# Optimization experiments

Measured on AMD Instinct MI355X. Metric: run time of the kernel, lower is better.

## Reference

```python
import jax, jax.numpy as jnp
import numpy as np

B = 262144
IN = 89          # obs(39) + one-hot task(50)
H = 64           # hidden_size
OUT = 8          # output_size
T = 50           # num_tasks


def setup_inputs() -> dict:
    key = jax.random.key(0)
    ks = jax.random.split(key, 10)
    s = 1.0 / np.sqrt(H)
    inputs = jax.random.normal(ks[0], (B, IN), dtype=jnp.float32)
    task_indices = jax.random.randint(ks[1], (B,), 0, T, dtype=jnp.int32)
    # trunk: 3 Linear+Tanh layers
    W0 = jax.random.normal(ks[2], (IN, H), dtype=jnp.float32) / np.sqrt(IN)
    b0 = jnp.zeros((H,), dtype=jnp.float32)
    W1 = jax.random.normal(ks[3], (H, H), dtype=jnp.float32) * s
    b1 = jnp.zeros((H,), dtype=jnp.float32)
    W2 = jax.random.normal(ks[4], (H, H), dtype=jnp.float32) * s
    b2 = jnp.zeros((H,), dtype=jnp.float32)
    # per-task output heads: num_task_layers=1 -> single Linear (no tanh)
    head_W = jax.random.normal(ks[5], (T, H, OUT), dtype=jnp.float32) * s
    head_b = jnp.zeros((T, OUT), dtype=jnp.float32)
    return {"inputs": inputs, "task_indices": task_indices,
            "W0": W0, "b0": b0, "W1": W1, "b1": b1, "W2": W2, "b2": b2,
            "head_W": head_W, "head_b": head_b}


def reference(inputs, task_indices, W0, b0, W1, b1, W2, b2, head_W, head_b):
    # Shared trunk: Linear + Tanh x3
    h = jnp.tanh(inputs @ W0 + b0)   # [B, H]
    h = jnp.tanh(h @ W1 + b1)
    h = jnp.tanh(h @ W2 + b2)
    # MoE-style dispatch/combine: gather per-sample head weights and apply.
    # Mathematically identical to partitioning by task, applying each head,
    # and scattering results back to original order.
    Wg = head_W[task_indices]        # [B, H, OUT]
    bg = head_b[task_indices]        # [B, OUT]
    out = jnp.einsum('bh,bho->bo', h, Wg) + bg  # [B, OUT]
    return out
```

## Files before the change

### kernel.cpp

```cpp
#include <hip/hip_runtime.h>
#include <stdint.h>
#include <stddef.h>


typedef _Float16 half8 __attribute__((ext_vector_type(8)));
typedef _Float16 half4 __attribute__((ext_vector_type(4)));
typedef _Float16 half2v __attribute__((ext_vector_type(2)));
typedef float    f32x4 __attribute__((ext_vector_type(4)));

constexpr int BN = 262144, INF = 89, HID = 64, OUTF = 8, NTASK = 50;
constexpr int NTHR = 512;
constexpr int NW   = 8;
constexpr int ROWS = 256;
constexpr int HP   = 72;
constexpr int WLF  = 14336;

constexpr int W0F_OFF = 0;
constexpr int W1F_OFF = 12288;
constexpr int W2F_OFF = 20480;
constexpr int HWT_OFF = 28672;

__device__ __forceinline__ float fast_tanh(float v) {
    float e = __expf(2.0f * v);
    return 1.0f - 2.0f * __builtin_amdgcn_rcpf(e + 1.0f);
}

__device__ __forceinline__ float dot2acc(half2v a, half2v b, float c) {
#if __has_builtin(__builtin_amdgcn_fdot2)
    return __builtin_amdgcn_fdot2(a, b, c, false);
#else
    return fmaf((float)a[0], (float)b[0], fmaf((float)a[1], (float)b[1], c));
#endif
}

__global__ void prep_kernel(const float* __restrict__ W0, const float* __restrict__ W1,
                            const float* __restrict__ W2, const float* __restrict__ hW,
                            _Float16* __restrict__ ws) {
    const int tid = blockIdx.x * blockDim.x + threadIdx.x;
    const int stride = gridDim.x * blockDim.x;
    _Float16* w0f = ws + W0F_OFF / 2;
    _Float16* w1f = ws + W1F_OFF / 2;
    _Float16* w2f = ws + W2F_OFF / 2;
    _Float16* hwt = ws + HWT_OFF / 2;
    for (int i = tid; i < 3 * 4 * 64 * 8; i += stride) {
        int j = i & 7, l = (i >> 3) & 63, fk = i >> 9;
        int kk = fk >> 2, ft = fk & 3;
        int n = ft * 16 + (l & 15);
        int g = l >> 4;
        bool tail = (kk == 2 && g == 3);
        int k = (tail ? 81 : kk * 32 + g * 8) + j;
        float wv = W0[k * HID + n];
        if (tail && j < 7) wv = 0.0f;
        w0f[i] = (_Float16)wv;
    }
    for (int i = tid; i < 2 * 4 * 64 * 8; i += stride) {
        int j = i & 7, l = (i >> 3) & 63, fk = i >> 9;
        int kk = fk >> 2, ft = fk & 3;
        int n = ft * 16 + (l & 15);
        int k = kk * 32 + (l >> 4) * 8 + j;
        w1f[i] = (_Float16)W1[k * HID + n];
        w2f[i] = (_Float16)W2[k * HID + n];
    }
    for (int i = tid; i < NTASK * OUTF * HID; i += stride) {
        int t = i / (OUTF * HID), rem = i % (OUTF * HID);
        int o = rem / HID, k = rem % HID;
        hwt[i] = (_Float16)hW[(size_t)t * (HID * OUTF) + k * OUTF + o];
    }
}

__global__ __launch_bounds__(NTHR, 4) void mtn_mfma_kernel(
    const float* __restrict__ x,
    const int*   __restrict__ task,
    const float* __restrict__ b0, const float* __restrict__ b1,
    const float* __restrict__ b2,
    const float* __restrict__ hB,
    const _Float16* __restrict__ ws,
    float* __restrict__ out)
{
    __shared__ __align__(16) _Float16 wl[WLF];
    __shared__ __align__(16) _Float16 hs[NW][32][HP];

    const int t = threadIdx.x;
    const int w = t >> 6;
    const int l = t & 63;
    const int c = l & 15;
    const int g = l >> 4;
    const int waveRow = blockIdx.x * ROWS + w * 32;

    const _Float16* hwt = ws + HWT_OFF / 2;

    {
        const float4* src = reinterpret_cast<const float4*>(ws);
        float4* dst = reinterpret_cast<float4*>(wl);
        #pragma unroll
        for (int i = 0; i < 3; ++i) dst[t + i * NTHR] = src[t + i * NTHR];
        if (t < 1792 - 3 * NTHR) dst[t + 3 * NTHR] = src[t + 3 * NTHR];
    }

    const int k0_2 = (g == 3) ? 81 : 64 + g * 8;
    half8 xf[3][2];
    #pragma unroll
    for (int bt = 0; bt < 2; ++bt) {
        const float* xr = x + (size_t)(waveRow + bt * 16 + c) * INF;
        #pragma unroll
        for (int kk = 0; kk < 3; ++kk) {
            const int k0 = (kk == 2) ? k0_2 : kk * 32 + g * 8;
            float v[8];
            __builtin_memcpy(v, xr + k0, 32);
            half8 hb;
            #pragma unroll
            for (int i2 = 0; i2 < 8; ++i2) hb[i2] = (_Float16)v[i2];
            xf[kk][bt] = hb;
        }
    }

    const int jr = l >> 3, jo = l & 7;
    int   tks[4];
    float hBv[4];
    #pragma unroll
    for (int it = 0; it < 4; ++it)
        tks[it] = task[waveRow + it * 8 + jr];
    #pragma unroll
    for (int it = 0; it < 4; ++it)
        hBv[it] = hB[tks[it] * OUTF + jo];

    __syncthreads();

    const _Float16* w0l = wl;
    const _Float16* w1l = wl + W1F_OFF / 2;
    const _Float16* w2l = wl + W2F_OFF / 2;

    f32x4 acc[4][2];

    #pragma unroll
    for (int ft = 0; ft < 4; ++ft) {
        f32x4 bv = *(const f32x4*)(b0 + ft * 16 + g * 4);
        acc[ft][0] = bv; acc[ft][1] = bv;
    }
    #pragma unroll
    for (int kk = 0; kk < 3; ++kk)
        #pragma unroll
        for (int ft = 0; ft < 4; ++ft) {
            half8 af = *(const half8*)(w0l + ((kk * 4 + ft) * 64 + l) * 8);
            acc[ft][0] = __builtin_amdgcn_mfma_f32_16x16x32_f16(af, xf[kk][0], acc[ft][0], 0, 0, 0);
            acc[ft][1] = __builtin_amdgcn_mfma_f32_16x16x32_f16(af, xf[kk][1], acc[ft][1], 0, 0, 0);
        }
    #pragma unroll
    for (int ft = 0; ft < 4; ++ft)
        #pragma unroll
        for (int bt = 0; bt < 2; ++bt) {
            half4 hv;
            #pragma unroll
            for (int r = 0; r < 4; ++r) hv[r] = (_Float16)fast_tanh(acc[ft][bt][r]);
            *(half4*)&hs[w][bt * 16 + c][ft * 16 + g * 4] = hv;
        }

    #pragma unroll
    for (int layer = 0; layer < 2; ++layer) {
        const _Float16* WL  = layer ? w2l : w1l;
        const float*    bia = layer ? b2  : b1;
        #pragma unroll
        for (int ft = 0; ft < 4; ++ft) {
            f32x4 bv = *(const f32x4*)(bia + ft * 16 + g * 4);
            acc[ft][0] = bv; acc[ft][1] = bv;
        }
        #pragma unroll
        for (int kk = 0; kk < 2; ++kk) {
            half8 bf[2];
            #pragma unroll
            for (int bt = 0; bt < 2; ++bt)
                bf[bt] = *(const half8*)&hs[w][bt * 16 + c][kk * 32 + g * 8];
            #pragma unroll
            for (int ft = 0; ft < 4; ++ft) {
                half8 af = *(const half8*)(WL + ((kk * 4 + ft) * 64 + l) * 8);
                acc[ft][0] = __builtin_amdgcn_mfma_f32_16x16x32_f16(af, bf[0], acc[ft][0], 0, 0, 0);
                acc[ft][1] = __builtin_amdgcn_mfma_f32_16x16x32_f16(af, bf[1], acc[ft][1], 0, 0, 0);
            }
        }
        #pragma unroll
        for (int ft = 0; ft < 4; ++ft)
            #pragma unroll
            for (int bt = 0; bt < 2; ++bt) {
                half4 hv;
                #pragma unroll
                for (int r = 0; r < 4; ++r) hv[r] = (_Float16)fast_tanh(acc[ft][bt][r]);
                *(half4*)&hs[w][bt * 16 + c][ft * 16 + g * 4] = hv;
            }
    }

    #pragma unroll
    for (int it = 0; it < 4; ++it) {
        const int r = it * 8 + jr;
        const size_t grow = (size_t)waveRow + r;
        const int tk = tks[it];
        const _Float16* wp = hwt + (size_t)tk * (OUTF * HID) + jo * 8;
        const half8 hv = *(const half8*)&hs[w][r][jo * 8];

        float p[8];
        #pragma unroll
        for (int o = 0; o < 8; ++o) {
            half8 wv = *(const half8*)(wp + o * HID);
            float a = 0.0f;
            #pragma unroll
            for (int pp = 0; pp < 4; ++pp) {
                half2v av = {hv[2 * pp], hv[2 * pp + 1]};
                half2v bv = {wv[2 * pp], wv[2 * pp + 1]};
                a = dot2acc(av, bv, a);
            }
            p[o] = a;
        }
        float t0 = p[0] + __shfl_xor(p[0], 1);
        float t1 = p[1] + __shfl_xor(p[1], 1);
        float t2 = p[2] + __shfl_xor(p[2], 1);
        float t3 = p[3] + __shfl_xor(p[3], 1);
        float t4 = p[4] + __shfl_xor(p[4], 1);
        float t5 = p[5] + __shfl_xor(p[5], 1);
        float t6 = p[6] + __shfl_xor(p[6], 1);
        float t7 = p[7] + __shfl_xor(p[7], 1);
        const bool b0s = (jo & 1) != 0;
        float s0 = b0s ? t1 : t0;
        float s1 = b0s ? t3 : t2;
        float s2 = b0s ? t5 : t4;
        float s3 = b0s ? t7 : t6;
        s0 += __shfl_xor(s0, 2);
        s1 += __shfl_xor(s1, 2);
        s2 += __shfl_xor(s2, 2);
        s3 += __shfl_xor(s3, 2);
        const bool b1s = (jo & 2) != 0;
        float u0 = b1s ? s1 : s0;
        float u1 = b1s ? s3 : s2;
        u0 += __shfl_xor(u0, 4);
        u1 += __shfl_xor(u1, 4);
        float res = ((jo & 4) ? u1 : u0) + hBv[it];
        out[grow * OUTF + jo] = res;
    }
}

extern "C" void kernel_launch(void* const* d_in, const int* in_sizes, int n_in,
                              void* d_out, int out_size, void* d_ws, size_t ws_size,
                              hipStream_t stream) {
    const float* x    = (const float*)d_in[0];
    const int*   task = (const int*)  d_in[1];
    const float* W0   = (const float*)d_in[2];
    const float* b0   = (const float*)d_in[3];
    const float* W1   = (const float*)d_in[4];
    const float* b1   = (const float*)d_in[5];
    const float* W2   = (const float*)d_in[6];
    const float* b2   = (const float*)d_in[7];
    const float* hW   = (const float*)d_in[8];
    const float* hB   = (const float*)d_in[9];
    float* out = (float*)d_out;
    _Float16* ws = (_Float16*)d_ws;

    prep_kernel<<<64, 256, 0, stream>>>(W0, W1, W2, hW, ws);
    mtn_mfma_kernel<<<BN / ROWS, NTHR, 0, stream>>>(x, task, b0, b1, b2, hB, ws, out);
}
```

Before: 39.75 us.

## Counting-sort rows by task before trunk kernel and gather through index

Adds a four-kernel counting sort (init, histogram, prefix, scatter) that builds a permutation grouping rows by task index. The main kernel then reads x rows, task ids and output positions through that permutation, so each wave mostly sees a single task's head weights. The aim is more uniform, cache-friendly head-weight access. In exchange it adds several extra launches and global atomics, and it turns the x reads and output writes into scattered gathers. If the workspace is too small, an identity index is used instead.

```diff
diff --git a/kernel.cpp b/kernel.cpp
--- a/kernel.cpp
+++ b/kernel.cpp
@@ -15,10 +15,14 @@
 constexpr int HP   = 72;
 constexpr int WLF  = 14336;
 
-constexpr int W0F_OFF = 0;
-constexpr int W1F_OFF = 12288;
-constexpr int W2F_OFF = 20480;
-constexpr int HWT_OFF = 28672;
+constexpr int    W0F_OFF  = 0;
+constexpr int    W1F_OFF  = 12288;
+constexpr int    W2F_OFF  = 20480;
+constexpr int    HWT_OFF  = 28672;
+constexpr size_t IDX_OFF  = 79872;
+constexpr size_t HIST_OFF = IDX_OFF + (size_t)BN * 4;
+constexpr size_t BASE_OFF = HIST_OFF + 256;
+constexpr size_t WS_NEED  = BASE_OFF + 256;
 
 __device__ __forceinline__ float fast_tanh(float v) {
     float e = __expf(2.0f * v);
@@ -68,9 +72,63 @@
     }
 }
 
+__global__ void sort_init(int* __restrict__ hist, int* __restrict__ base) {
+    int t = threadIdx.x;
+    if (t < 64) { hist[t] = 0; base[t] = 0; }
+}
+
+__global__ __launch_bounds__(256) void sort_hist(const int* __restrict__ task,
+                                                 int* __restrict__ hist) {
+    __shared__ int lh[NTASK];
+    const int t = threadIdx.x;
+    if (t < NTASK) lh[t] = 0;
+    __syncthreads();
+    const int base = blockIdx.x * 1024;
+    #pragma unroll
+    for (int k = 0; k < 4; ++k) atomicAdd(&lh[task[base + t + k * 256]], 1);
+    __syncthreads();
+    if (t < NTASK) atomicAdd(&hist[t], lh[t]);
+}
+
+__global__ void sort_prefix(const int* __restrict__ hist, int* __restrict__ base) {
+    if (threadIdx.x == 0) {
+        int run = 0;
+        for (int i = 0; i < NTASK; ++i) { base[i] = run; run += hist[i]; }
+    }
+}
+
+__global__ __launch_bounds__(256) void sort_scatter(const int* __restrict__ task,
+                                                    int* __restrict__ base,
+                                                    int* __restrict__ idx) {
+    __shared__ int lcnt[NTASK];
+    __shared__ int lbase[NTASK];
+    const int t = threadIdx.x;
+    if (t < NTASK) lcnt[t] = 0;
+    __syncthreads();
+    const int rbase = blockIdx.x * 1024;
+    int tk[4], rank[4];
+    #pragma unroll
+    for (int k = 0; k < 4; ++k) {
+        tk[k] = task[rbase + t + k * 256];
+        rank[k] = atomicAdd(&lcnt[tk[k]], 1);
+    }
+    __syncthreads();
+    if (t < NTASK) lbase[t] = atomicAdd(&base[t], lcnt[t]);
+    __syncthreads();
+    #pragma unroll
+    for (int k = 0; k < 4; ++k)
+        idx[lbase[tk[k]] + rank[k]] = rbase + t + k * 256;
+}
+
+__global__ void idx_identity(int* __restrict__ idx) {
+    int i = blockIdx.x * blockDim.x + threadIdx.x;
+    idx[i] = i;
+}
+
 __global__ __launch_bounds__(NTHR, 4) void mtn_mfma_kernel(
     const float* __restrict__ x,
     const int*   __restrict__ task,
+    const int*   __restrict__ idx,
     const float* __restrict__ b0, const float* __restrict__ b1,
     const float* __restrict__ b2,
     const float* __restrict__ hB,
@@ -97,11 +155,16 @@
         if (t < 1792 - 3 * NTHR) dst[t + 3 * NTHR] = src[t + 3 * NTHR];
     }
 
+    int rowT[2];
+    #pragma unroll
+    for (int bt = 0; bt < 2; ++bt)
+        rowT[bt] = idx[waveRow + bt * 16 + c];
+
     const int k0_2 = (g == 3) ? 81 : 64 + g * 8;
     half8 xf[3][2];
     #pragma unroll
     for (int bt = 0; bt < 2; ++bt) {
-        const float* xr = x + (size_t)(waveRow + bt * 16 + c) * INF;
+        const float* xr = x + (size_t)rowT[bt] * INF;
         #pragma unroll
         for (int kk = 0; kk < 3; ++kk) {
             const int k0 = (kk == 2) ? k0_2 : kk * 32 + g * 8;
@@ -115,11 +178,14 @@
     }
 
     const int jr = l >> 3, jo = l & 7;
-    int   tks[4];
+    int   rowH[4], tks[4];
     float hBv[4];
     #pragma unroll
     for (int it = 0; it < 4; ++it)
-        tks[it] = task[waveRow + it * 8 + jr];
+        rowH[it] = idx[waveRow + it * 8 + jr];
+    #pragma unroll
+    for (int it = 0; it < 4; ++it)
+        tks[it] = task[rowH[it]];
     #pragma unroll
     for (int it = 0; it < 4; ++it)
         hBv[it] = hB[tks[it] * OUTF + jo];
@@ -191,7 +257,7 @@
     #pragma unroll
     for (int it = 0; it < 4; ++it) {
         const int r = it * 8 + jr;
-        const size_t grow = (size_t)waveRow + r;
+        const size_t grow = (size_t)rowH[it];
         const int tk = tks[it];
         const _Float16* wp = hwt + (size_t)tk * (OUTF * HID) + jo * 8;
         const half8 hv = *(const half8*)&hs[w][r][jo * 8];
@@ -251,7 +317,22 @@
     const float* hB   = (const float*)d_in[9];
     float* out = (float*)d_out;
     _Float16* ws = (_Float16*)d_ws;
+    char* wsb = (char*)d_ws;
+    int* idx = (int*)(wsb + IDX_OFF);
 
     prep_kernel<<<64, 256, 0, stream>>>(W0, W1, W2, hW, ws);
-    mtn_mfma_kernel<<<BN / ROWS, NTHR, 0, stream>>>(x, task, b0, b1, b2, hB, ws, out);
-}
+
+    if (ws_size >= WS_NEED) {
+        int* hist = (int*)(wsb + HIST_OFF);
+        int* base = (int*)(wsb + BASE_OFF);
+        sort_init   <<<1,   128, 0, stream>>>(hist, base);
+        sort_hist   <<<256, 256, 0, stream>>>(task, hist);
+        sort_prefix <<<1,    64, 0, stream>>>(hist, base);
+        sort_scatter<<<256, 256, 0, stream>>>(task, base, idx);
+    } else {
+        idx_identity<<<BN / 256, 256, 0, stream>>>(idx);
+    }
+
+    mtn_mfma_kernel<<<BN / ROWS, NTHR, 0, stream>>>(x, task, idx, b0, b1, b2,
+                                                    hB, ws, out);
+}
```

Result: slower. 65.60 us (+65.1%).
